# Kernel optimization log

Hardware: AMD Instinct MI355X
Metric: run time of the kernel (lower is better)

The kernel has to match this reference:

```python
import jax, jax.numpy as jnp
import numpy as np

N_NODES = 100_000
N_EDGES = 1_600_000  # avg degree 16
D_FEAT = 64


def setup_inputs() -> dict:
    key = jax.random.key(0)
    k_x, k_val, k_src, k_dst = jax.random.split(key, 4)
    x = jax.random.normal(k_x, (N_NODES, D_FEAT), dtype=jnp.float32)
    edge_val = jax.random.uniform(k_val, (N_EDGES,), dtype=jnp.float32)
    edge_src = jax.random.randint(k_src, (N_EDGES,), 0, N_NODES, dtype=jnp.int32)
    edge_dst = jax.random.randint(k_dst, (N_EDGES,), 0, N_NODES, dtype=jnp.int32)
    return {"x": x, "edge_val": edge_val, "edge_src": edge_src, "edge_dst": edge_dst}


def reference(x, edge_val, edge_src, edge_dst):
    # out = adj @ x  with adj in COO form:
    # out[dst] += val * x[src]   (sparse-dense matmul, SpMM)
    msgs = x[edge_src] * edge_val[:, None]          # [E, D] gather + scale
    out = jax.ops.segment_sum(msgs, edge_dst, num_segments=N_NODES)  # [N, D] scatter-add
    return out
```

## Files before the change

kernel.cpp:

```cpp
#include <hip/hip_runtime.h>

#define N_NODES 100000
#define N_EDGES 1600000
#define D_FEAT 64
#define NPB 128
#define K_BUCKETS 782
#define CAP 2304
#define A_BLOCKS 400
#define A_CHUNK 4000

__global__ void scatterA(const int* __restrict__ src, const int* __restrict__ dst,
                         const float* __restrict__ val, int* __restrict__ cursor,
                         int2* __restrict__ bdata) {
    __shared__ int sh_cnt[K_BUCKETS];
    __shared__ int sh_base[K_BUCKETS];
    for (int i = threadIdx.x; i < K_BUCKETS; i += 256) sh_cnt[i] = 0;
    __syncthreads();
    const int base = blockIdx.x * A_CHUNK;
    for (int j = threadIdx.x; j < A_CHUNK; j += 256)
        atomicAdd(&sh_cnt[dst[base + j] >> 7], 1);
    __syncthreads();
    for (int i = threadIdx.x; i < K_BUCKETS; i += 256) {
        const int c = sh_cnt[i];
        sh_base[i] = c ? (i * CAP + atomicAdd(&cursor[i], c)) : 0;
    }
    __syncthreads();
    for (int i = threadIdx.x; i < K_BUCKETS; i += 256) sh_cnt[i] = 0;
    __syncthreads();
    for (int j = threadIdx.x; j < A_CHUNK; j += 256) {
        const int e = base + j;
        const int d = dst[e];
        const int b = d >> 7;
        const int slot = atomicAdd(&sh_cnt[b], 1);
        bdata[sh_base[b] + slot] =
            make_int2(src[e] | ((d & 127) << 17), __float_as_int(val[e]));
    }
}

__global__ void sortB(int2* __restrict__ bdata, const int* __restrict__ cursor,
                      int* __restrict__ rbeg, int* __restrict__ rdeg) {
    __shared__ int2 sh_e[CAP];
    __shared__ int cnt[NPB];
    __shared__ int cur[NPB];
    const int b = blockIdx.x;
    const int count = min(cursor[b], CAP);
    const int base = b * CAP;
    const int t = threadIdx.x;
    if (t < NPB) cnt[t] = 0;
    __syncthreads();
    for (int j = t; j < count; j += 256) {
        const int2 e = bdata[base + j];
        sh_e[j] = e;
        atomicAdd(&cnt[e.x >> 17], 1);
    }
    __syncthreads();
    const int v = (t < NPB) ? cnt[t] : 0;
    for (int off = 1; off < NPB; off <<= 1) {
        int u = 0;
        if (t < NPB && t >= off) u = cnt[t - off];
        __syncthreads();
        if (t < NPB) cnt[t] += u;
        __syncthreads();
    }
    const int row0 = b * NPB;
    if (t < NPB) {
        const int excl = cnt[t] - v;
        cur[t] = excl;
        if (row0 + t < N_NODES) { rbeg[row0 + t] = base + excl; rdeg[row0 + t] = v; }
    }
    __syncthreads();
    for (int j = t; j < count; j += 256) {
        const int2 pv = sh_e[j];
        const int dl = pv.x >> 17;
        const int slot = atomicAdd(&cur[dl], 1);
        bdata[base + slot] = make_int2(pv.x & 0x1FFFF, pv.y);
    }
}

__global__ void spmm_csr(const float* __restrict__ x,
                         const int* __restrict__ rbeg,
                         const int* __restrict__ rdeg,
                         const int2* __restrict__ csr,
                         float* __restrict__ out) {
    const int tid = blockIdx.x * blockDim.x + threadIdx.x;
    const int row = tid >> 4;
    const int c = tid & 15;
    if (row >= N_NODES) return;
    const int beg = rbeg[row];
    const int end = beg + rdeg[row];
    float4 acc = {0.f, 0.f, 0.f, 0.f};
    int j = beg;
    for (; j + 2 <= end; j += 2) {
        const int2 p0 = csr[j];
        const int2 p1 = csr[j + 1];
        const float4 m0 = ((const float4*)(x + (size_t)p0.x * D_FEAT))[c];
        const float4 m1 = ((const float4*)(x + (size_t)p1.x * D_FEAT))[c];
        const float v0 = __int_as_float(p0.y);
        const float v1 = __int_as_float(p1.y);
        acc.x += v0 * m0.x + v1 * m1.x;
        acc.y += v0 * m0.y + v1 * m1.y;
        acc.z += v0 * m0.z + v1 * m1.z;
        acc.w += v0 * m0.w + v1 * m1.w;
    }
    if (j < end) {
        const int2 p0 = csr[j];
        const float4 m0 = ((const float4*)(x + (size_t)p0.x * D_FEAT))[c];
        const float v0 = __int_as_float(p0.y);
        acc.x += v0 * m0.x;
        acc.y += v0 * m0.y;
        acc.z += v0 * m0.z;
        acc.w += v0 * m0.w;
    }
    ((float4*)(out + (size_t)row * D_FEAT))[c] = acc;
}

extern "C" void kernel_launch(void* const* d_in, const int* in_sizes, int n_in,
                              void* d_out, int out_size, void* d_ws, size_t ws_size,
                              hipStream_t stream) {
    const float* x        = (const float*)d_in[0];
    const float* edge_val = (const float*)d_in[1];
    const int*   edge_src = (const int*)d_in[2];
    const int*   edge_dst = (const int*)d_in[3];
    float* out = (float*)d_out;

    int* ws     = (int*)d_ws;
    int* cursor = ws;
    int* rbeg   = cursor + K_BUCKETS;
    int* rdeg   = rbeg + N_NODES;
    size_t used = (size_t)K_BUCKETS + 2 * N_NODES;
    used = (used + 1) & ~(size_t)1;
    int2* bdata = (int2*)(ws + used);

    hipMemsetAsync(cursor, 0, K_BUCKETS * sizeof(int), stream);

    const int B = 256;
    const int gridRow = (N_NODES * 16 + B - 1) / B;

    scatterA<<<A_BLOCKS, 256, 0, stream>>>(edge_src, edge_dst, edge_val, cursor, bdata);
    sortB   <<<K_BUCKETS, 256, 0, stream>>>(bdata, cursor, rbeg, rdeg);
    spmm_csr<<<gridRow, B, 0, stream>>>(x, rbeg, rdeg, bdata, out);
}
```

Baseline: 202.7 us.

## Fuse bucket sort and SpMM into one kernel using shared-memory CSR

Merges the per-bucket sort and the SpMM into a single kernel. Sorted edges now stay in LDS instead of being written back to global memory and re-read, and the rbeg/rdeg arrays are dropped. Each block processes its 128 rows with 16 row groups, and the gather loop is unrolled by 4. The scatter kernel also moves to 512 threads per block. In exchange, SpMM parallelism drops to 782 blocks with about 37KB of LDS each, which may lower occupancy, and a single block's rows run serially across its row groups.

```diff
diff --git a/kernel.cpp b/kernel.cpp
--- a/kernel.cpp
+++ b/kernel.cpp
@@ -8,26 +8,28 @@
 #define CAP 2304
 #define A_BLOCKS 400
 #define A_CHUNK 4000
+#define A_THREADS 512
 
-__global__ void scatterA(const int* __restrict__ src, const int* __restrict__ dst,
-                         const float* __restrict__ val, int* __restrict__ cursor,
-                         int2* __restrict__ bdata) {
+__global__ __launch_bounds__(A_THREADS) void scatterA(
+        const int* __restrict__ src, const int* __restrict__ dst,
+        const float* __restrict__ val, int* __restrict__ cursor,
+        int2* __restrict__ bdata) {
     __shared__ int sh_cnt[K_BUCKETS];
     __shared__ int sh_base[K_BUCKETS];
-    for (int i = threadIdx.x; i < K_BUCKETS; i += 256) sh_cnt[i] = 0;
+    for (int i = threadIdx.x; i < K_BUCKETS; i += A_THREADS) sh_cnt[i] = 0;
     __syncthreads();
     const int base = blockIdx.x * A_CHUNK;
-    for (int j = threadIdx.x; j < A_CHUNK; j += 256)
+    for (int j = threadIdx.x; j < A_CHUNK; j += A_THREADS)
         atomicAdd(&sh_cnt[dst[base + j] >> 7], 1);
     __syncthreads();
-    for (int i = threadIdx.x; i < K_BUCKETS; i += 256) {
+    for (int i = threadIdx.x; i < K_BUCKETS; i += A_THREADS) {
         const int c = sh_cnt[i];
         sh_base[i] = c ? (i * CAP + atomicAdd(&cursor[i], c)) : 0;
     }
     __syncthreads();
-    for (int i = threadIdx.x; i < K_BUCKETS; i += 256) sh_cnt[i] = 0;
+    for (int i = threadIdx.x; i < K_BUCKETS; i += A_THREADS) sh_cnt[i] = 0;
     __syncthreads();
-    for (int j = threadIdx.x; j < A_CHUNK; j += 256) {
+    for (int j = threadIdx.x; j < A_CHUNK; j += A_THREADS) {
         const int e = base + j;
         const int d = dst[e];
         const int b = d >> 7;
@@ -37,15 +39,18 @@
     }
 }
 
-__global__ void sortB(int2* __restrict__ bdata, const int* __restrict__ cursor,
-                      int* __restrict__ rbeg, int* __restrict__ rdeg) {
+__global__ __launch_bounds__(256) void sort_spmm(
+        const float* __restrict__ x, const int2* __restrict__ bdata,
+        const int* __restrict__ cursor, float* __restrict__ out) {
     __shared__ int2 sh_e[CAP];
+    __shared__ int2 sh_s[CAP];
     __shared__ int cnt[NPB];
     __shared__ int cur[NPB];
     const int b = blockIdx.x;
     const int count = min(cursor[b], CAP);
     const int base = b * CAP;
     const int t = threadIdx.x;
+
     if (t < NPB) cnt[t] = 0;
     __syncthreads();
     for (int j = t; j < count; j += 256) {
@@ -62,56 +67,55 @@
         if (t < NPB) cnt[t] += u;
         __syncthreads();
     }
-    const int row0 = b * NPB;
-    if (t < NPB) {
-        const int excl = cnt[t] - v;
-        cur[t] = excl;
-        if (row0 + t < N_NODES) { rbeg[row0 + t] = base + excl; rdeg[row0 + t] = v; }
-    }
+    if (t < NPB) cur[t] = cnt[t] - v;
     __syncthreads();
     for (int j = t; j < count; j += 256) {
         const int2 pv = sh_e[j];
         const int dl = pv.x >> 17;
         const int slot = atomicAdd(&cur[dl], 1);
-        bdata[base + slot] = make_int2(pv.x & 0x1FFFF, pv.y);
+        sh_s[slot] = make_int2(pv.x & 0x1FFFF, pv.y);
     }
-}
+    __syncthreads();
 
-__global__ void spmm_csr(const float* __restrict__ x,
-                         const int* __restrict__ rbeg,
-                         const int* __restrict__ rdeg,
-                         const int2* __restrict__ csr,
-                         float* __restrict__ out) {
-    const int tid = blockIdx.x * blockDim.x + threadIdx.x;
-    const int row = tid >> 4;
-    const int c = tid & 15;
-    if (row >= N_NODES) return;
-    const int beg = rbeg[row];
-    const int end = beg + rdeg[row];
-    float4 acc = {0.f, 0.f, 0.f, 0.f};
-    int j = beg;
-    for (; j + 2 <= end; j += 2) {
-        const int2 p0 = csr[j];
-        const int2 p1 = csr[j + 1];
-        const float4 m0 = ((const float4*)(x + (size_t)p0.x * D_FEAT))[c];
-        const float4 m1 = ((const float4*)(x + (size_t)p1.x * D_FEAT))[c];
-        const float v0 = __int_as_float(p0.y);
-        const float v1 = __int_as_float(p1.y);
-        acc.x += v0 * m0.x + v1 * m1.x;
-        acc.y += v0 * m0.y + v1 * m1.y;
-        acc.z += v0 * m0.z + v1 * m1.z;
-        acc.w += v0 * m0.w + v1 * m1.w;
+    const int lane = t & 15;
+    const int rg = t >> 4;
+    const int row0 = b * NPB;
+    for (int r = rg; r < NPB; r += 16) {
+        const int node = row0 + r;
+        if (node >= N_NODES) continue;
+        const int beg = r ? cnt[r - 1] : 0;
+        const int end = cnt[r];
+        float4 acc = {0.f, 0.f, 0.f, 0.f};
+        int j = beg;
+        for (; j + 4 <= end; j += 4) {
+            const int2 p0 = sh_s[j];
+            const int2 p1 = sh_s[j + 1];
+            const int2 p2 = sh_s[j + 2];
+            const int2 p3 = sh_s[j + 3];
+            const float4 m0 = ((const float4*)(x + (size_t)p0.x * D_FEAT))[lane];
+            const float4 m1 = ((const float4*)(x + (size_t)p1.x * D_FEAT))[lane];
+            const float4 m2 = ((const float4*)(x + (size_t)p2.x * D_FEAT))[lane];
+            const float4 m3 = ((const float4*)(x + (size_t)p3.x * D_FEAT))[lane];
+            const float v0 = __int_as_float(p0.y);
+            const float v1 = __int_as_float(p1.y);
+            const float v2 = __int_as_float(p2.y);
+            const float v3 = __int_as_float(p3.y);
+            acc.x += v0 * m0.x + v1 * m1.x + v2 * m2.x + v3 * m3.x;
+            acc.y += v0 * m0.y + v1 * m1.y + v2 * m2.y + v3 * m3.y;
+            acc.z += v0 * m0.z + v1 * m1.z + v2 * m2.z + v3 * m3.z;
+            acc.w += v0 * m0.w + v1 * m1.w + v2 * m2.w + v3 * m3.w;
+        }
+        for (; j < end; ++j) {
+            const int2 p0 = sh_s[j];
+            const float4 m0 = ((const float4*)(x + (size_t)p0.x * D_FEAT))[lane];
+            const float v0 = __int_as_float(p0.y);
+            acc.x += v0 * m0.x;
+            acc.y += v0 * m0.y;
+            acc.z += v0 * m0.z;
+            acc.w += v0 * m0.w;
+        }
+        ((float4*)(out + (size_t)node * D_FEAT))[lane] = acc;
     }
-    if (j < end) {
-        const int2 p0 = csr[j];
-        const float4 m0 = ((const float4*)(x + (size_t)p0.x * D_FEAT))[c];
-        const float v0 = __int_as_float(p0.y);
-        acc.x += v0 * m0.x;
-        acc.y += v0 * m0.y;
-        acc.z += v0 * m0.z;
-        acc.w += v0 * m0.w;
-    }
-    ((float4*)(out + (size_t)row * D_FEAT))[c] = acc;
 }
 
 extern "C" void kernel_launch(void* const* d_in, const int* in_sizes, int n_in,
@@ -125,18 +129,11 @@
 
     int* ws     = (int*)d_ws;
     int* cursor = ws;
-    int* rbeg   = cursor + K_BUCKETS;
-    int* rdeg   = rbeg + N_NODES;
-    size_t used = (size_t)K_BUCKETS + 2 * N_NODES;
-    used = (used + 1) & ~(size_t)1;
-    int2* bdata = (int2*)(ws + used);
+    int2* bdata = (int2*)(ws + K_BUCKETS);
 
     hipMemsetAsync(cursor, 0, K_BUCKETS * sizeof(int), stream);
 
-    const int B = 256;
-    const int gridRow = (N_NODES * 16 + B - 1) / B;
-
-    scatterA<<<A_BLOCKS, 256, 0, stream>>>(edge_src, edge_dst, edge_val, cursor, bdata);
-    sortB   <<<K_BUCKETS, 256, 0, stream>>>(bdata, cursor, rbeg, rdeg);
-    spmm_csr<<<gridRow, B, 0, stream>>>(x, rbeg, rdeg, bdata, out);
+    scatterA <<<A_BLOCKS, A_THREADS, 0, stream>>>(edge_src, edge_dst, edge_val,
+                                                  cursor, bdata);
+    sort_spmm<<<K_BUCKETS, 256, 0, stream>>>(x, bdata, cursor, out);
 }
```

Result: faster. 182.0 us (-10.2%).
